# Kernel optimization log

Hardware: AMD Instinct MI355X
Metric: run time of the kernel (lower is better)

The kernel has to match this reference:

```python
import jax, jax.numpy as jnp
import numpy as np

B, M, C = 8, 8192, 256   # batch, seeds, seed feature dim
F = 128                  # vote feature dim
P, K = 256, 32           # proposals, samples per group
CA, NCLS = 256, 10       # aggregated feat dim, classes
RADIUS = 0.3


def _lin(x, w, b):
    # 1x1 conv == pointwise linear; w: (out, in)
    return jnp.einsum('...c,oc->...o', x, w) + b


def _bnrelu(x, s, t):
    # eval-mode BatchNorm folded to per-channel affine, then ReLU
    return jnp.maximum(x * s + t, 0.0)


def _fps(xyz, npoint):
    # farthest point sampling; deterministic start at index 0
    Bb, N, _ = xyz.shape
    bidx = jnp.arange(Bb)

    def step(carry, _):
        distance, farthest = carry
        centroid = xyz[bidx, farthest][:, None, :]          # (B,1,2)
        d = jnp.sum((xyz - centroid) ** 2, -1)              # (B,N)
        distance = jnp.minimum(distance, d)
        return (distance, jnp.argmax(distance, -1)), farthest

    init = (jnp.full((Bb, N), 1e10, xyz.dtype), jnp.zeros((Bb,), jnp.int32))
    _, idx = jax.lax.scan(step, init, None, length=npoint)
    return jnp.transpose(idx)                               # (B, npoint)


def _ball_query(xyz, new_xyz, radius, nsample):
    # squared-distance cdist (monotone in euclid dist, so same sort order)
    N = xyz.shape[1]
    d2 = (jnp.sum(new_xyz ** 2, -1)[:, :, None]
          + jnp.sum(xyz ** 2, -1)[:, None, :]
          - 2.0 * jnp.einsum('bsd,bnd->bsn', new_xyz, xyz))  # (B,S,N)
    gidx = jnp.broadcast_to(jnp.arange(N), d2.shape)
    # out-of-radius points replaced by group_first (= index 0, as in source)
    gidx = jnp.where(d2 > radius * radius, 0, gidx)
    order = jnp.argsort(d2, axis=-1)
    return jnp.take_along_axis(gidx, order, axis=-1)[:, :, :nsample]


def _gather(points, idx):
    # points: (B,N,C); idx: (B,...) -> (B,...,C)
    return jax.vmap(lambda p, i: p[i])(points, idx)


def _forward(seed_xyz, seed_feats,
             v_off_w1, v_off_b1, v_off_s1, v_off_t1, v_off_w2, v_off_b2,
             v_ft_w1, v_ft_b1, v_ft_s1, v_ft_t1, v_ft_w2, v_ft_b2,
             a_w1, a_b1, a_s1, a_t1, a_w2, a_b2, a_s2, a_t2,
             p_w1, p_b1, p_s1, p_t1, p_w2, p_b2, p_s2, p_t2,
             obj_w, obj_b, cls_w, cls_b):
    # --- VotingModule (vote_factor=1) ---
    h = _bnrelu(_lin(seed_feats, v_off_w1, v_off_b1), v_off_s1, v_off_t1)
    offsets = _lin(h, v_off_w2, v_off_b2)                   # (B,M,2)
    g = _bnrelu(_lin(seed_feats, v_ft_w1, v_ft_b1), v_ft_s1, v_ft_t1)
    vote_feats = _lin(g, v_ft_w2, v_ft_b2)                  # (B,M,F)
    votes_xyz = seed_xyz + offsets                          # (B,M,2)

    # --- VoteAggregation ---
    fps_idx = _fps(votes_xyz, P)                            # (B,P)
    new_xyz = _gather(votes_xyz, fps_idx)                   # (B,P,2)
    gidx = _ball_query(votes_xyz, new_xyz, RADIUS, K)       # (B,P,K)
    gv = _gather(votes_xyz, gidx)                           # (B,P,K,2)
    gf = _gather(vote_feats, gidx)                          # (B,P,K,F)
    comb = jnp.concatenate([gv - new_xyz[:, :, None, :], gf], -1)  # (B,P,K,F+2)
    x = _bnrelu(_lin(comb, a_w1, a_b1), a_s1, a_t1)
    x = _bnrelu(_lin(x, a_w2, a_b2), a_s2, a_t2)
    pooled = jnp.max(x, axis=2)                             # (B,P,CA)

    # --- ProposalHead ---
    y = _bnrelu(_lin(pooled, p_w1, p_b1), p_s1, p_t1)
    y = _bnrelu(_lin(y, p_w2, p_b2), p_s2, p_t2)
    obj = _lin(y, obj_w, obj_b)[..., 0]                     # (B,P)
    cls = _lin(y, cls_w, cls_b)                             # (B,P,NCLS)
    return (new_xyz, obj, cls)


def setup_inputs() -> dict:
    key = jax.random.key(0)
    keys = iter(jax.random.split(key, 40))

    def w(shape):
        return (jax.random.normal(next(keys), shape) * 0.05).astype(jnp.float32)

    inp = {
        'seed_xyz': jax.random.uniform(next(keys), (B, M, 2), jnp.float32),
        'seed_feats': jax.random.normal(next(keys), (B, M, C), jnp.float32),
        # voting: offset branch
        'v_off_w1': w((C, C)), 'v_off_b1': w((C,)),
        'v_off_s1': 1.0 + w((C,)), 'v_off_t1': w((C,)),
        'v_off_w2': w((2, C)), 'v_off_b2': w((2,)),
        # voting: feature branch
        'v_ft_w1': w((C, C)), 'v_ft_b1': w((C,)),
        'v_ft_s1': 1.0 + w((C,)), 'v_ft_t1': w((C,)),
        'v_ft_w2': w((F, C)), 'v_ft_b2': w((F,)),
        # aggregation MLP
        'a_w1': w((CA, F + 2)), 'a_b1': w((CA,)),
        'a_s1': 1.0 + w((CA,)), 'a_t1': w((CA,)),
        'a_w2': w((CA, CA)), 'a_b2': w((CA,)),
        'a_s2': 1.0 + w((CA,)), 'a_t2': w((CA,)),
        # proposal head
        'p_w1': w((CA, CA)), 'p_b1': w((CA,)),
        'p_s1': 1.0 + w((CA,)), 'p_t1': w((CA,)),
        'p_w2': w((CA // 2, CA)), 'p_b2': w((CA // 2,)),
        'p_s2': 1.0 + w((CA // 2,)), 'p_t2': w((CA // 2,)),
        'obj_w': w((1, CA // 2)), 'obj_b': w((1,)),
        'cls_w': w((NCLS, CA // 2)), 'cls_b': w((NCLS,)),
    }
    return inp


def reference(seed_xyz, seed_feats,
              v_off_w1, v_off_b1, v_off_s1, v_off_t1, v_off_w2, v_off_b2,
              v_ft_w1, v_ft_b1, v_ft_s1, v_ft_t1, v_ft_w2, v_ft_b2,
              a_w1, a_b1, a_s1, a_t1, a_w2, a_b2, a_s2, a_t2,
              p_w1, p_b1, p_s1, p_t1, p_w2, p_b2, p_s2, p_t2,
              obj_w, obj_b, cls_w, cls_b):
    return _forward(seed_xyz, seed_feats,
                    v_off_w1, v_off_b1, v_off_s1, v_off_t1, v_off_w2, v_off_b2,
                    v_ft_w1, v_ft_b1, v_ft_s1, v_ft_t1, v_ft_w2, v_ft_b2,
                    a_w1, a_b1, a_s1, a_t1, a_w2, a_b2, a_s2, a_t2,
                    p_w1, p_b1, p_s1, p_t1, p_w2, p_b2, p_s2, p_t2,
                    obj_w, obj_b, cls_w, cls_b)
```

## Files before the change

kernel.cpp:

```cpp
#include <hip/hip_runtime.h>

typedef __attribute__((ext_vector_type(8))) short bf16x8;
typedef __attribute__((ext_vector_type(4))) float f32x4;
typedef unsigned short u16;
typedef unsigned int u32;
typedef unsigned long long u64;

#define DEV static __device__ __forceinline__
DEV u16 f2bf(float f) { u32 i = __float_as_uint(f); i += 0x7fffu + ((i >> 16) & 1u); return (u16)(i >> 16); }
DEV float bf2f(u16 u) { return __uint_as_float(((u32)u) << 16); }

constexpr int Mn = 8192;
constexpr int Pn = 256;
constexpr int Kn = 32;
constexpr float R2 = 0.09f;

__global__ __launch_bounds__(256) void k_voting_off(
    const float* __restrict__ sxyz,
    const float* __restrict__ sfeat,
    const float* __restrict__ ow1, const float* __restrict__ ob1,
    const float* __restrict__ os1, const float* __restrict__ ot1,
    const float* __restrict__ ow2, const float* __restrict__ ob2,
    float* __restrict__ votes)
{
  __shared__ float Xst[256][17];
  __shared__ float Hst[256][17];
  __shared__ float Wc[16][260];

  const int tid = threadIdx.x;
  const int row0 = blockIdx.x * 16;

  for (int i = tid; i < 16 * 256; i += 256) {
    int r = i >> 8, c = i & 255;
    Xst[c][r] = sfeat[(row0 + r) * 256 + c];
  }
  __syncthreads();

  const int rg = tid >> 6;
  const int ro = rg * 4;
  const int cg = tid & 63;

  float acc[4][4];
#pragma unroll
  for (int r = 0; r < 4; ++r)
#pragma unroll
    for (int j = 0; j < 4; ++j) acc[r][j] = 0.f;
  const int co = cg * 4;

  for (int kc = 0; kc < 16; ++kc) {
    __syncthreads();
    for (int i = tid; i < 256 * 16; i += 256) {
      int o = i >> 4, k = i & 15;
      Wc[k][o] = ow1[o * 256 + kc * 16 + k];
    }
    __syncthreads();
#pragma unroll
    for (int k = 0; k < 16; ++k) {
      const int kk = kc * 16 + k;
      float x[4], w[4];
#pragma unroll
      for (int r = 0; r < 4; ++r) x[r] = Xst[kk][ro + r];
#pragma unroll
      for (int j = 0; j < 4; ++j) w[j] = Wc[k][co + j];
#pragma unroll
      for (int r = 0; r < 4; ++r)
#pragma unroll
        for (int j = 0; j < 4; ++j)
          acc[r][j] = fmaf(x[r], w[j], acc[r][j]);
    }
  }
  __syncthreads();
#pragma unroll
  for (int j = 0; j < 4; ++j) {
    int o = co + j;
    float bb = ob1[o], ss = os1[o], tt = ot1[o];
#pragma unroll
    for (int r = 0; r < 4; ++r)
      Hst[o][ro + r] = fmaxf((acc[r][j] + bb) * ss + tt, 0.f);
  }
  __syncthreads();

  if (tid < 32) {
    int r = tid >> 1, o = tid & 1;
    float a = 0.f;
    for (int k = 0; k < 256; ++k)
      a = fmaf(Hst[k][r], ow2[o * 256 + k], a);
    a += ob2[o];
    int row = row0 + r;
    votes[row * 2 + o] = sxyz[row * 2 + o] + a;
  }
}

__global__ __launch_bounds__(512, 1) void k_fps(
    const float* __restrict__ votes, float* __restrict__ nxyz,
    float* __restrict__ out)
{
  const int b = blockIdx.x, tid = threadIdx.x;
  const float* vb = votes + b * Mn * 2;
  __shared__ uint4 slots[2][32];
  __shared__ float histx[256], histy[256];

  float px[16], py[16], dist[16];
#pragma unroll
  for (int s = 0; s < 16; ++s) {
    int i = tid * 16 + s;
    float2 p = *(const float2*)&vb[i * 2];
    px[s] = p.x; py[s] = p.y; dist[s] = 1e10f;
  }
  float cx = vb[0], cy = vb[1];
  if (tid == 0) { histx[0] = cx; histy[0] = cy; }

  for (int it = 1; it < Pn; ++it) {
    float bd = -1.f; float bx = 0.f, by = 0.f; int bi = 0;
#pragma unroll
    for (int s = 0; s < 16; ++s) {
      float dx = px[s] - cx, dy = py[s] - cy;
      float d = fminf(dist[s], dx * dx + dy * dy);
      dist[s] = d;
      if (d > bd) { bd = d; bi = tid * 16 + s; bx = px[s]; by = py[s]; }
    }
    u32 hd = __float_as_uint(bd), hl = ~(u32)bi;
    u32 hx = __float_as_uint(bx), hy = __float_as_uint(by);

#define FPS_ROR(N)                                                              \
    {                                                                           \
      u32 od = (u32)__builtin_amdgcn_update_dpp(0, (int)hd, 0x120 + N, 0xF, 0xF, false); \
      u32 ol = (u32)__builtin_amdgcn_update_dpp(0, (int)hl, 0x120 + N, 0xF, 0xF, false); \
      u32 ox = (u32)__builtin_amdgcn_update_dpp(0, (int)hx, 0x120 + N, 0xF, 0xF, false); \
      u32 oy = (u32)__builtin_amdgcn_update_dpp(0, (int)hy, 0x120 + N, 0xF, 0xF, false); \
      bool g = (od > hd) || (od == hd && ol > hl);                              \
      hd = g ? od : hd; hl = g ? ol : hl; hx = g ? ox : hx; hy = g ? oy : hy;   \
    }
    FPS_ROR(8) FPS_ROR(4) FPS_ROR(2) FPS_ROR(1)

    const int buf = it & 1;
    if ((tid & 15) == 0) slots[buf][tid >> 4] = make_uint4(hd, hl, hx, hy);
    __syncthreads();

    uint4 t0 = slots[buf][tid & 15];
    uint4 t1 = slots[buf][16 + (tid & 15)];
    {
      bool g = (t1.x > t0.x) || (t1.x == t0.x && t1.y > t0.y);
      if (g) t0 = t1;
    }
    u32 rd = t0.x, rl = t0.y, rx = t0.z, ry = t0.w;
#define FPS_ROR2(N)                                                             \
    {                                                                           \
      u32 od = (u32)__builtin_amdgcn_update_dpp(0, (int)rd, 0x120 + N, 0xF, 0xF, false); \
      u32 ol = (u32)__builtin_amdgcn_update_dpp(0, (int)rl, 0x120 + N, 0xF, 0xF, false); \
      u32 ox = (u32)__builtin_amdgcn_update_dpp(0, (int)rx, 0x120 + N, 0xF, 0xF, false); \
      u32 oy = (u32)__builtin_amdgcn_update_dpp(0, (int)ry, 0x120 + N, 0xF, 0xF, false); \
      bool g = (od > rd) || (od == rd && ol > rl);                              \
      rd = g ? od : rd; rl = g ? ol : rl; rx = g ? ox : rx; ry = g ? oy : ry;   \
    }
    FPS_ROR2(8) FPS_ROR2(4) FPS_ROR2(2) FPS_ROR2(1)
#undef FPS_ROR
#undef FPS_ROR2

    cx = __uint_as_float(rx); cy = __uint_as_float(ry);
    if (tid == 0) { histx[it] = cx; histy[it] = cy; }
  }
  __syncthreads();
  if (tid < 256) {
    float2 o2; o2.x = histx[tid]; o2.y = histy[tid];
    *(float2*)&nxyz[(b * Pn + tid) * 2] = o2;
    *(float2*)&out[(b * Pn + tid) * 2] = o2;
  }
}

__global__ __launch_bounds__(256) void k_ballq(
    const float* __restrict__ votes, const float* __restrict__ nxyz,
    int* __restrict__ gidx)
{
  const int bp = blockIdx.x, tid = threadIdx.x;
  const int b = bp >> 8;
  const float* vb = votes + b * Mn * 2;
  const float sx = nxyz[bp * 2], sy = nxyz[bp * 2 + 1];
  const float a = sx * sx + sy * sy;
  float d2[32];
#pragma unroll
  for (int s = 0; s < 32; ++s) {
    int i = tid * 32 + s;
    float x = vb[i * 2], y = vb[i * 2 + 1];
    d2[s] = (a + (x * x + y * y)) - 2.f * (sx * x + sy * y);
  }
  __shared__ float sd[4];
  __shared__ int si[4];
  __shared__ int swi;
  unsigned mask = 0;
  for (int kk = 0; kk < Kn; ++kk) {
    float bd = 3.4e38f; int bi = 0x7fffffff;
#pragma unroll
    for (int s = 0; s < 32; ++s)
      if (!((mask >> s) & 1u) && d2[s] < bd) { bd = d2[s]; bi = tid * 32 + s; }
#pragma unroll
    for (int off = 32; off > 0; off >>= 1) {
      float od = __shfl_xor(bd, off);
      int oi = __shfl_xor(bi, off);
      if (od < bd || (od == bd && oi < bi)) { bd = od; bi = oi; }
    }
    if ((tid & 63) == 0) { sd[tid >> 6] = bd; si[tid >> 6] = bi; }
    __syncthreads();
    if (tid == 0) {
#pragma unroll
      for (int w = 1; w < 4; ++w)
        if (sd[w] < bd || (sd[w] == bd && si[w] < bi)) { bd = sd[w]; bi = si[w]; }
      swi = bi;
      gidx[bp * Kn + kk] = (bd > R2) ? 0 : bi;
    }
    __syncthreads();
    int wi = swi;
    if ((wi >> 5) == tid) mask |= 1u << (wi & 31);
  }
}

__global__ __launch_bounds__(256) void k_prep(
    const float* __restrict__ fw1, const float* __restrict__ fw2,
    const float* __restrict__ aw1, const float* __restrict__ aw2,
    u16* __restrict__ FW1h, u16* __restrict__ FW2b,
    u16* __restrict__ AW1b, u16* __restrict__ AW2b)
{
  const int gid = blockIdx.x * 256 + threadIdx.x;
  const int gsz = gridDim.x * 256;
  for (int i = gid; i < 65536; i += gsz) FW1h[i] = f2bf(fw1[i]);
  for (int i = gid; i < 32768; i += gsz) FW2b[i] = f2bf(fw2[i]);
  for (int i = gid; i < 65536; i += gsz) AW2b[i] = f2bf(aw2[i]);
  for (int i = gid; i < 49152; i += gsz) {
    int o = i / 192, k = i % 192;
    AW1b[i] = (k < 130) ? f2bf(aw1[o * 130 + k]) : (u16)0;
  }
}

__global__ __launch_bounds__(256) void k_vf(
    const float* __restrict__ sfeat, const u16* __restrict__ FW1h,
    const float* __restrict__ fb1, const float* __restrict__ fs1,
    const float* __restrict__ ft1, const u16* __restrict__ FW2b,
    const float* __restrict__ fb2, u16* __restrict__ vfeat)
{
  __shared__ u16 Hs[128 * 136];
  __shared__ u16 As[128 * 40];
  __shared__ u16 Bs[128 * 40];
  const int tid = threadIdx.x;
  const int row0 = blockIdx.x * 128;
  const int wid = tid >> 6, lane = tid & 63, m16 = lane & 15, quad = lane >> 4;
  const int wr = wid >> 1, wc = wid & 1;
  const int sr = tid >> 1, sk = (tid & 1) * 16;

  f32x4 acc2[4][4];
#pragma unroll
  for (int mt = 0; mt < 4; ++mt)
#pragma unroll
    for (int nt = 0; nt < 4; ++nt) acc2[mt][nt] = (f32x4){0.f, 0.f, 0.f, 0.f};

  for (int h = 0; h < 2; ++h) {
    f32x4 acc[4][4];
#pragma unroll
    for (int mt = 0; mt < 4; ++mt)
#pragma unroll
      for (int nt = 0; nt < 4; ++nt) acc[mt][nt] = (f32x4){0.f, 0.f, 0.f, 0.f};

    for (int s = 0; s < 8; ++s) {
      __syncthreads();
      {
        const float* src = &sfeat[(row0 + sr) * 256 + s * 32 + sk];
        u32 packed[8];
#pragma unroll
        for (int q = 0; q < 4; ++q) {
          float4 v = *(const float4*)&src[q * 4];
          packed[q * 2]     = (u32)f2bf(v.x) | ((u32)f2bf(v.y) << 16);
          packed[q * 2 + 1] = (u32)f2bf(v.z) | ((u32)f2bf(v.w) << 16);
        }
        *(uint4*)&As[sr * 40 + sk]     = *(uint4*)&packed[0];
        *(uint4*)&As[sr * 40 + sk + 8] = *(uint4*)&packed[4];
        const u16* bsrc = &FW1h[(h * 128 + sr) * 256 + s * 32 + sk];
        *(uint4*)&Bs[sr * 40 + sk]     = *(const uint4*)&bsrc[0];
        *(uint4*)&Bs[sr * 40 + sk + 8] = *(const uint4*)&bsrc[8];
      }
      __syncthreads();
#pragma unroll
      for (int mt = 0; mt < 4; ++mt) {
        bf16x8 af = *(const bf16x8*)&As[(wr * 64 + mt * 16 + m16) * 40 + quad * 8];
#pragma unroll
        for (int nt = 0; nt < 4; ++nt) {
          bf16x8 bfr = *(const bf16x8*)&Bs[(wc * 64 + nt * 16 + m16) * 40 + quad * 8];
          acc[mt][nt] = __builtin_amdgcn_mfma_f32_16x16x32_bf16(af, bfr, acc[mt][nt], 0, 0, 0);
        }
      }
    }
    __syncthreads();
#pragma unroll
    for (int nt = 0; nt < 4; ++nt) {
      int colL = wc * 64 + nt * 16 + m16;
      int col = h * 128 + colL;
      float bb = fb1[col], ss = fs1[col], tt = ft1[col];
#pragma unroll
      for (int mt = 0; mt < 4; ++mt) {
        int rL = wr * 64 + mt * 16 + quad * 4;
#pragma unroll
        for (int r = 0; r < 4; ++r)
          Hs[(rL + r) * 136 + colL] = f2bf(fmaxf((acc[mt][nt][r] + bb) * ss + tt, 0.f));
      }
    }
    for (int s2 = 0; s2 < 4; ++s2) {
      __syncthreads();
      {
        const u16* bsrc = &FW2b[sr * 256 + h * 128 + s2 * 32 + sk];
        *(uint4*)&Bs[sr * 40 + sk]     = *(const uint4*)&bsrc[0];
        *(uint4*)&Bs[sr * 40 + sk + 8] = *(const uint4*)&bsrc[8];
      }
      __syncthreads();
#pragma unroll
      for (int mt = 0; mt < 4; ++mt) {
        bf16x8 af = *(const bf16x8*)&Hs[(wr * 64 + mt * 16 + m16) * 136 + s2 * 32 + quad * 8];
#pragma unroll
        for (int nt = 0; nt < 4; ++nt) {
          bf16x8 bfr = *(const bf16x8*)&Bs[(wc * 64 + nt * 16 + m16) * 40 + quad * 8];
          acc2[mt][nt] = __builtin_amdgcn_mfma_f32_16x16x32_bf16(af, bfr, acc2[mt][nt], 0, 0, 0);
        }
      }
    }
  }
#pragma unroll
  for (int nt = 0; nt < 4; ++nt) {
    int col = wc * 64 + nt * 16 + m16;
    float bb = fb2[col];
#pragma unroll
    for (int mt = 0; mt < 4; ++mt) {
      int rbase = row0 + wr * 64 + mt * 16 + quad * 4;
#pragma unroll
      for (int r = 0; r < 4; ++r)
        vfeat[(rbase + r) * 128 + col] = f2bf(acc2[mt][nt][r] + bb);
    }
  }
}

__global__ __launch_bounds__(256) void k_agg(
    const float* __restrict__ votes, const u16* __restrict__ vfeat,
    const float* __restrict__ nxyz, const int* __restrict__ gidx,
    const u16* __restrict__ AW1b, const float* __restrict__ ab1,
    const float* __restrict__ as1, const float* __restrict__ at1,
    const u16* __restrict__ AW2b, const float* __restrict__ ab2,
    const float* __restrict__ as2, const float* __restrict__ at2,
    float* __restrict__ pooled)
{
  __shared__ u16 U[32 * 264];
  __shared__ u16 Bs[256 * 72];
  __shared__ int gix[32];
  __shared__ float gvx[32], gvy[32];
  u16* CombA = U;
  u16* As = U;
  float* x2T = (float*)Bs;

  const int bp = blockIdx.x, tid = threadIdx.x, b = bp >> 8;
  if (tid < 32) {
    int g = gidx[bp * 32 + tid];
    gix[tid] = g;
    gvx[tid] = votes[(b * Mn + g) * 2];
    gvy[tid] = votes[(b * Mn + g) * 2 + 1];
  }
  __syncthreads();
  const float sx = nxyz[bp * 2], sy = nxyz[bp * 2 + 1];

  if (tid < 192) {
    int row = tid / 6, c = tid % 6;
    const u16* vsrc = &vfeat[(b * Mn + gix[row]) * 128];
    u16* dst = &CombA[row * 200 + c * 32];
    if (c == 0) {
      dst[0] = f2bf(gvx[row] - sx);
      dst[1] = f2bf(gvy[row] - sy);
      for (int k = 2; k < 32; ++k) dst[k] = vsrc[k - 2];
    } else if (c <= 3) {
      for (int k = 0; k < 32; ++k) dst[k] = vsrc[c * 32 + k - 2];
    } else if (c == 4) {
      dst[0] = vsrc[126]; dst[1] = vsrc[127];
      for (int k = 2; k < 32; ++k) dst[k] = 0;
    } else {
      for (int k = 0; k < 32; ++k) dst[k] = 0;
    }
  }

  const int wid = tid >> 6, lane = tid & 63, m16 = lane & 15, quad = lane >> 4;
  const int mt = wid & 1, nh = wid >> 1;

  f32x4 acc[8];
#pragma unroll
  for (int nt = 0; nt < 8; ++nt) acc[nt] = (f32x4){0.f, 0.f, 0.f, 0.f};
  for (int s = 0; s < 3; ++s) {
    __syncthreads();
    for (int i = tid; i < 4096; i += 256) {
      int n = i >> 4, c4 = i & 15;
      *(uint2*)&Bs[n * 72 + c4 * 4] = *(const uint2*)&AW1b[n * 192 + s * 64 + c4 * 4];
    }
    __syncthreads();
#pragma unroll
    for (int ks = 0; ks < 2; ++ks) {
      bf16x8 af = *(const bf16x8*)&CombA[(mt * 16 + m16) * 200 + s * 64 + ks * 32 + quad * 8];
#pragma unroll
      for (int nt = 0; nt < 8; ++nt) {
        bf16x8 bf_ = *(const bf16x8*)&Bs[(nh * 128 + nt * 16 + m16) * 72 + ks * 32 + quad * 8];
        acc[nt] = __builtin_amdgcn_mfma_f32_16x16x32_bf16(af, bf_, acc[nt], 0, 0, 0);
      }
    }
  }
  __syncthreads();
#pragma unroll
  for (int nt = 0; nt < 8; ++nt) {
    int col = nh * 128 + nt * 16 + m16;
    float bb = ab1[col], ss = as1[col], tt = at1[col];
#pragma unroll
    for (int r = 0; r < 4; ++r) {
      int samp = mt * 16 + quad * 4 + r;
      As[samp * 264 + col] = f2bf(fmaxf((acc[nt][r] + bb) * ss + tt, 0.f));
    }
  }

  f32x4 acc2[8];
#pragma unroll
  for (int nt = 0; nt < 8; ++nt) acc2[nt] = (f32x4){0.f, 0.f, 0.f, 0.f};
  for (int s = 0; s < 4; ++s) {
    __syncthreads();
    for (int i = tid; i < 4096; i += 256) {
      int n = i >> 4, c4 = i & 15;
      *(uint2*)&Bs[n * 72 + c4 * 4] = *(const uint2*)&AW2b[n * 256 + s * 64 + c4 * 4];
    }
    __syncthreads();
#pragma unroll
    for (int ks = 0; ks < 2; ++ks) {
      bf16x8 af = *(const bf16x8*)&As[(mt * 16 + m16) * 264 + s * 64 + ks * 32 + quad * 8];
#pragma unroll
      for (int nt = 0; nt < 8; ++nt) {
        bf16x8 bf_ = *(const bf16x8*)&Bs[(nh * 128 + nt * 16 + m16) * 72 + ks * 32 + quad * 8];
        acc2[nt] = __builtin_amdgcn_mfma_f32_16x16x32_bf16(af, bf_, acc2[nt], 0, 0, 0);
      }
    }
  }
  __syncthreads();
#pragma unroll
  for (int nt = 0; nt < 8; ++nt) {
    int col = nh * 128 + nt * 16 + m16;
    float bb = ab2[col], ss = as2[col], tt = at2[col];
#pragma unroll
    for (int r = 0; r < 4; ++r) {
      int samp = mt * 16 + quad * 4 + r;
      x2T[col * 33 + samp] = fmaxf((acc2[nt][r] + bb) * ss + tt, 0.f);
    }
  }
  __syncthreads();
  {
    float m = x2T[tid * 33];
#pragma unroll
    for (int s2 = 1; s2 < 32; ++s2) m = fmaxf(m, x2T[tid * 33 + s2]);
    pooled[bp * 256 + tid] = m;
  }
}

__global__ __launch_bounds__(256) void k_head(
    const float* __restrict__ pooled,
    const float* __restrict__ pw1, const float* __restrict__ pb1,
    const float* __restrict__ ps1, const float* __restrict__ pt1,
    const float* __restrict__ pw2, const float* __restrict__ pb2,
    const float* __restrict__ ps2, const float* __restrict__ pt2,
    const float* __restrict__ objw, const float* __restrict__ objb,
    const float* __restrict__ clsw, const float* __restrict__ clsb,
    float* __restrict__ out)
{
  __shared__ float xr[256], y1[256], y2[128];
  const int bp = blockIdx.x, tid = threadIdx.x;
  xr[tid] = pooled[bp * 256 + tid];
  __syncthreads();
  {
    float a = 0.f;
    for (int c = 0; c < 256; ++c) a = fmaf(xr[c], pw1[tid * 256 + c], a);
    a = (a + pb1[tid]) * ps1[tid] + pt1[tid];
    y1[tid] = fmaxf(a, 0.f);
  }
  __syncthreads();
  if (tid < 128) {
    float a = 0.f;
    for (int c = 0; c < 256; ++c) a = fmaf(y1[c], pw2[tid * 256 + c], a);
    a = (a + pb2[tid]) * ps2[tid] + pt2[tid];
    y2[tid] = fmaxf(a, 0.f);
  }
  __syncthreads();
  if (tid < 10) {
    float a = 0.f;
    for (int c = 0; c < 128; ++c) a = fmaf(y2[c], clsw[tid * 128 + c], a);
    out[6144 + bp * 10 + tid] = a + clsb[tid];
  } else if (tid == 10) {
    float a = 0.f;
    for (int c = 0; c < 128; ++c) a = fmaf(y2[c], objw[c], a);
    out[4096 + bp] = a + objb[0];
  }
}

extern "C" void kernel_launch(void* const* d_in, const int* in_sizes, int n_in,
                              void* d_out, int out_size, void* d_ws, size_t ws_size,
                              hipStream_t stream)
{
  (void)in_sizes; (void)n_in; (void)out_size; (void)ws_size;
  const float* sxyz  = (const float*)d_in[0];
  const float* sfeat = (const float*)d_in[1];
  const float* ow1 = (const float*)d_in[2];
  const float* ob1 = (const float*)d_in[3];
  const float* os1 = (const float*)d_in[4];
  const float* ot1 = (const float*)d_in[5];
  const float* ow2 = (const float*)d_in[6];
  const float* ob2 = (const float*)d_in[7];
  const float* fw1 = (const float*)d_in[8];
  const float* fb1 = (const float*)d_in[9];
  const float* fs1 = (const float*)d_in[10];
  const float* ft1 = (const float*)d_in[11];
  const float* fw2 = (const float*)d_in[12];
  const float* fb2 = (const float*)d_in[13];
  const float* aw1 = (const float*)d_in[14];
  const float* ab1 = (const float*)d_in[15];
  const float* as1 = (const float*)d_in[16];
  const float* at1 = (const float*)d_in[17];
  const float* aw2 = (const float*)d_in[18];
  const float* ab2 = (const float*)d_in[19];
  const float* as2 = (const float*)d_in[20];
  const float* at2 = (const float*)d_in[21];
  const float* pw1 = (const float*)d_in[22];
  const float* pb1 = (const float*)d_in[23];
  const float* ps1 = (const float*)d_in[24];
  const float* pt1 = (const float*)d_in[25];
  const float* pw2 = (const float*)d_in[26];
  const float* pb2 = (const float*)d_in[27];
  const float* ps2 = (const float*)d_in[28];
  const float* pt2 = (const float*)d_in[29];
  const float* objw = (const float*)d_in[30];
  const float* objb = (const float*)d_in[31];
  const float* clsw = (const float*)d_in[32];
  const float* clsb = (const float*)d_in[33];

  char* ws = (char*)d_ws;
  float* votes  = (float*)(ws + 0);
  u16*   vfeat  = (u16*)  (ws + 524288);
  float* nxyz   = (float*)(ws + 17301504);
  int*   gidxp  = (int*)  (ws + 17317888);
  float* pooled = (float*)(ws + 17580032);
  u16*   FW1h   = (u16*)  (ws + 19677184);
  u16*   FW2b   = (u16*)  (ws + 19808256);
  u16*   AW1b   = (u16*)  (ws + 19873792);
  u16*   AW2b   = (u16*)  (ws + 19972096);
  float* out    = (float*)d_out;

  k_voting_off<<<dim3(4096), dim3(256), 0, stream>>>(
      sxyz, sfeat, ow1, ob1, os1, ot1, ow2, ob2, votes);

  k_fps<<<dim3(8), dim3(512), 0, stream>>>(votes, nxyz, out);

  k_ballq<<<dim3(2048), dim3(256), 0, stream>>>(votes, nxyz, gidxp);

  k_prep<<<dim3(256), dim3(256), 0, stream>>>(
      fw1, fw2, aw1, aw2, FW1h, FW2b, AW1b, AW2b);

  k_vf<<<dim3(512), dim3(256), 0, stream>>>(
      sfeat, FW1h, fb1, fs1, ft1, FW2b, fb2, vfeat);

  k_agg<<<dim3(2048), dim3(256), 0, stream>>>(
      votes, vfeat, nxyz, gidxp, AW1b, ab1, as1, at1,
      AW2b, ab2, as2, at2, pooled);

  k_head<<<dim3(2048), dim3(256), 0, stream>>>(
      pooled, pw1, pb1, ps1, pt1, pw2, pb2, ps2, pt2,
      objw, objb, clsw, clsb, out);
}
```

Baseline: 1.032 ms.

## Stage FPS points in LDS and reduce only distance/index pairs

The FPS kernel now copies all votes of a batch into shared memory instead of holding them in registers. The argmax reduction carries only the distance and index, and the winning centroid coordinates are read back from LDS. Point ownership changes from contiguous to strided, so ties still break toward the lower index. This halves the DPP traffic per reduction step and frees registers, but adds an LDS read per point on every iteration plus a dependent LDS load for the centroid on the serial critical path.

```diff
diff --git a/kernel.cpp b/kernel.cpp
--- a/kernel.cpp
+++ b/kernel.cpp
@@ -97,67 +97,75 @@
 {
   const int b = blockIdx.x, tid = threadIdx.x;
   const float* vb = votes + b * Mn * 2;
-  __shared__ uint4 slots[2][32];
+  __shared__ float2 xy[Mn];
+  __shared__ u32 Sd[2][32], Sl[2][32];
   __shared__ float histx[256], histy[256];
 
-  float px[16], py[16], dist[16];
-#pragma unroll
-  for (int s = 0; s < 16; ++s) {
-    int i = tid * 16 + s;
-    float2 p = *(const float2*)&vb[i * 2];
-    px[s] = p.x; py[s] = p.y; dist[s] = 1e10f;
-  }
-  float cx = vb[0], cy = vb[1];
+  {
+    const float4* vb4 = (const float4*)vb;
+#pragma unroll
+    for (int j = tid; j < Mn / 2; j += 512) {
+      float4 v = vb4[j];
+      *(float4*)&xy[2 * j] = v;
+    }
+  }
+  float dist[16];
+#pragma unroll
+  for (int s = 0; s < 16; ++s) dist[s] = 1e10f;
+  __syncthreads();
+
+  float cx = xy[0].x, cy = xy[0].y;
   if (tid == 0) { histx[0] = cx; histy[0] = cy; }
 
   for (int it = 1; it < Pn; ++it) {
-    float bd = -1.f; float bx = 0.f, by = 0.f; int bi = 0;
+    float bd = -1.f; int sb = 0;
 #pragma unroll
     for (int s = 0; s < 16; ++s) {
-      float dx = px[s] - cx, dy = py[s] - cy;
+      float2 p = xy[s * 512 + tid];
+      float dx = p.x - cx, dy = p.y - cy;
       float d = fminf(dist[s], dx * dx + dy * dy);
       dist[s] = d;
-      if (d > bd) { bd = d; bi = tid * 16 + s; bx = px[s]; by = py[s]; }
-    }
+      if (d > bd) { bd = d; sb = s; }
+    }
+    int bi = sb * 512 + tid;
+
     u32 hd = __float_as_uint(bd), hl = ~(u32)bi;
-    u32 hx = __float_as_uint(bx), hy = __float_as_uint(by);
-
-#define FPS_ROR(N)                                                              \
+
+#define FPS_ROR(VD, VL, N)                                                      \
     {                                                                           \
-      u32 od = (u32)__builtin_amdgcn_update_dpp(0, (int)hd, 0x120 + N, 0xF, 0xF, false); \
-      u32 ol = (u32)__builtin_amdgcn_update_dpp(0, (int)hl, 0x120 + N, 0xF, 0xF, false); \
-      u32 ox = (u32)__builtin_amdgcn_update_dpp(0, (int)hx, 0x120 + N, 0xF, 0xF, false); \
-      u32 oy = (u32)__builtin_amdgcn_update_dpp(0, (int)hy, 0x120 + N, 0xF, 0xF, false); \
-      bool g = (od > hd) || (od == hd && ol > hl);                              \
-      hd = g ? od : hd; hl = g ? ol : hl; hx = g ? ox : hx; hy = g ? oy : hy;   \
-    }
-    FPS_ROR(8) FPS_ROR(4) FPS_ROR(2) FPS_ROR(1)
+      u32 od = (u32)__builtin_amdgcn_update_dpp(0, (int)VD, 0x120 + N, 0xF, 0xF, false); \
+      u32 ol = (u32)__builtin_amdgcn_update_dpp(0, (int)VL, 0x120 + N, 0xF, 0xF, false); \
+      bool g = (od > VD) || (od == VD && ol > VL);                              \
+      VD = g ? od : VD; VL = g ? ol : VL;                                       \
+    }
+    FPS_ROR(hd, hl, 8)
+    FPS_ROR(hd, hl, 4)
+    FPS_ROR(hd, hl, 2)
+    FPS_ROR(hd, hl, 1)
 
     const int buf = it & 1;
-    if ((tid & 15) == 0) slots[buf][tid >> 4] = make_uint4(hd, hl, hx, hy);
-    __syncthreads();
-
-    uint4 t0 = slots[buf][tid & 15];
-    uint4 t1 = slots[buf][16 + (tid & 15)];
+    if ((tid & 15) == 0) {
+      int row = tid >> 4;
+      Sd[buf][row] = hd; Sl[buf][row] = hl;
+    }
+    __syncthreads();
+
+    int rr = tid & 15;
+    u32 rd = Sd[buf][rr], rl = Sl[buf][rr];
     {
-      bool g = (t1.x > t0.x) || (t1.x == t0.x && t1.y > t0.y);
-      if (g) t0 = t1;
-    }
-    u32 rd = t0.x, rl = t0.y, rx = t0.z, ry = t0.w;
-#define FPS_ROR2(N)                                                             \
-    {                                                                           \
-      u32 od = (u32)__builtin_amdgcn_update_dpp(0, (int)rd, 0x120 + N, 0xF, 0xF, false); \
-      u32 ol = (u32)__builtin_amdgcn_update_dpp(0, (int)rl, 0x120 + N, 0xF, 0xF, false); \
-      u32 ox = (u32)__builtin_amdgcn_update_dpp(0, (int)rx, 0x120 + N, 0xF, 0xF, false); \
-      u32 oy = (u32)__builtin_amdgcn_update_dpp(0, (int)ry, 0x120 + N, 0xF, 0xF, false); \
-      bool g = (od > rd) || (od == rd && ol > rl);                              \
-      rd = g ? od : rd; rl = g ? ol : rl; rx = g ? ox : rx; ry = g ? oy : ry;   \
-    }
-    FPS_ROR2(8) FPS_ROR2(4) FPS_ROR2(2) FPS_ROR2(1)
+      u32 od = Sd[buf][16 + rr], ol = Sl[buf][16 + rr];
+      bool g = (od > rd) || (od == rd && ol > rl);
+      rd = g ? od : rd; rl = g ? ol : rl;
+    }
+    FPS_ROR(rd, rl, 8)
+    FPS_ROR(rd, rl, 4)
+    FPS_ROR(rd, rl, 2)
+    FPS_ROR(rd, rl, 1)
 #undef FPS_ROR
-#undef FPS_ROR2
-
-    cx = __uint_as_float(rx); cy = __uint_as_float(ry);
+
+    int widx = (int)(~rl);
+    float2 w = xy[widx];
+    cx = w.x; cy = w.y;
     if (tid == 0) { histx[it] = cx; histy[it] = cy; }
   }
   __syncthreads();
```

Result: faster. 947.5 us (-8.2%).
